# Optimization experiments

Hardware: AMD Instinct MI355X
Metric: run time of the kernel (lower is better)

## Reference

```python
import jax, jax.numpy as jnp
import numpy as np

EMBED_DIM = 1280
NUM_STATES = 20
B, L = 8, 1024

# upper-triangular (offset=1) indices, matching torch.triu_indices(N, N, offset=1)
_IU, _JU = np.triu_indices(NUM_STATES, k=1)


def setup_inputs() -> dict:
    key = jax.random.key(0)
    ks = jax.random.split(key, 4)
    d = EMBED_DIM
    n = NUM_STATES
    m = n * (n - 1) // 2
    s = 1.0 / np.sqrt(d)
    return {
        "hx": jax.random.normal(ks[0], (B, L, d), dtype=jnp.float32),
        "dense_w": jax.random.normal(ks[1], (d, d), dtype=jnp.float32) * s,
        "dense_b": jnp.zeros((d,), dtype=jnp.float32),
        "ln_w": jnp.ones((d,), dtype=jnp.float32),
        "ln_b": jnp.zeros((d,), dtype=jnp.float32),
        "theta_w": jax.random.normal(ks[2], (d, n), dtype=jnp.float32) * s,
        "theta_b": jnp.zeros((n,), dtype=jnp.float32),
        "Theta_w": jax.random.normal(ks[3], (d, m), dtype=jnp.float32) * s,
        "Theta_b": jnp.zeros((m,), dtype=jnp.float32),
    }


def _layer_norm(x, w, b, eps=1e-5):
    mu = jnp.mean(x, axis=-1, keepdims=True)
    var = jnp.mean(jnp.square(x - mu), axis=-1, keepdims=True)
    return (x - mu) * jax.lax.rsqrt(var + eps) * w + b


def reference(hx, dense_w, dense_b, ln_w, ln_b, theta_w, theta_b, Theta_w, Theta_b):
    n = NUM_STATES
    # dense -> exact gelu (ESM uses erf gelu) -> layer norm
    h = hx @ dense_w + dense_b                        # [B,L,D]
    h = _layer_norm(jax.nn.gelu(h, approximate=False), ln_w, ln_b)
    pi = jax.nn.softmax(h @ theta_w + theta_b, axis=-1)          # [B,L,N]
    Theta = jax.nn.softplus(h @ Theta_w + Theta_b)               # [B,L,N*(N-1)/2]
    # scatter upper triangle, then symmetrize
    S = jnp.zeros((*h.shape[:2], n, n), dtype=h.dtype).at[..., _IU, _JU].set(Theta)
    S = S + jnp.swapaxes(S, -2, -1)                              # [B,L,N,N]
    # diag(1/sqrt(pi)) @ S @ diag(sqrt(pi)) == elementwise row/col scaling
    pi_sqrt = jnp.sqrt(pi)
    Q = S * (pi_sqrt[..., None, :] / pi_sqrt[..., :, None])
    # Q - diag_embed(Q.sum(-1))
    Q = Q - Q.sum(axis=-1)[..., :, None] * jnp.eye(n, dtype=Q.dtype)
    return Q
```

## Files before the change

kernel.cpp:

```cpp
#include <hip/hip_runtime.h>
#include <hip/hip_bf16.h>
#include <math.h>

#define D 1280
#define NST 20
#define MTRI 190
#define NTOK 8192
#define NC 256

typedef __attribute__((ext_vector_type(4))) float f32x4;
typedef __attribute__((ext_vector_type(8))) __bf16 bf16x8;
typedef __attribute__((ext_vector_type(8))) unsigned short ushort8;
typedef __attribute__((ext_vector_type(4))) unsigned short bfu4;

__device__ __forceinline__ void gload_lds16(const void* g, void* l) {
    __builtin_amdgcn_global_load_lds(
        (const __attribute__((address_space(1))) void*)g,
        (__attribute__((address_space(3))) void*)l, 16, 0, 0);
}

__device__ __forceinline__ unsigned short f2bf(float x) {
    __hip_bfloat16 b = __float2bfloat16(x);
    return __builtin_bit_cast(unsigned short, b);
}
__device__ __forceinline__ float bf2f(unsigned short u) {
    unsigned int x = ((unsigned int)u) << 16;
    return __builtin_bit_cast(float, x);
}

__global__ __launch_bounds__(256) void tobf_kernel(
    const float* __restrict__ X, unsigned short* __restrict__ Y)
{
    const size_t i = ((size_t)blockIdx.x * 256 + threadIdx.x) * 8;
    float4 a = *(const float4*)(X + i);
    float4 b = *(const float4*)(X + i + 4);
    ushort8 u;
    u[0] = f2bf(a.x); u[1] = f2bf(a.y); u[2] = f2bf(a.z); u[3] = f2bf(a.w);
    u[4] = f2bf(b.x); u[5] = f2bf(b.y); u[6] = f2bf(b.z); u[7] = f2bf(b.w);
    *(ushort8*)(Y + i) = u;
}

__global__ __launch_bounds__(256) void transpose_w_kernel(
    const float* __restrict__ W, unsigned short* __restrict__ Wt)
{
    __shared__ float t[64][65];
    const int tid = threadIdx.x;
    const int k0 = blockIdx.x * 64, n0 = blockIdx.y * 64;
#pragma unroll
    for (int i = 0; i < 16; ++i) {
        int lin = i * 256 + tid;
        int r = lin >> 6, c = lin & 63;
        t[r][c] = W[(size_t)(k0 + r) * D + n0 + c];
    }
    __syncthreads();
#pragma unroll
    for (int i = 0; i < 16; ++i) {
        int lin = i * 256 + tid;
        int r = lin >> 6, c = lin & 63;
        Wt[(size_t)(n0 + r) * D + (k0 + c)] = f2bf(t[c][r]);
    }
}

__global__ __launch_bounds__(256) void build_wcat_kernel(
    const float* __restrict__ theta_w, const float* __restrict__ Theta_w,
    unsigned short* __restrict__ Wcat)
{
    const int col = threadIdx.x;
    const int k0  = blockIdx.x * 64;
    for (int kk = 0; kk < 64; kk += 8) {
        ushort8 u;
#pragma unroll
        for (int j = 0; j < 8; ++j) {
            int k = k0 + kk + j;
            float v = 0.0f;
            if (col < NST)             v = theta_w[(size_t)k * NST + col];
            else if (col < NST + MTRI) v = Theta_w[(size_t)k * MTRI + (col - NST)];
            u[j] = f2bf(v);
        }
        *(ushort8*)&Wcat[(size_t)col * D + k0 + kk] = u;
    }
}

#define BKA 32

__global__ __launch_bounds__(256) void gemm_gelu_mfma_kernel(
    const unsigned short* __restrict__ Ab,
    const unsigned short* __restrict__ Wt,
    const float* __restrict__ bias,
    unsigned short* __restrict__ H)
{
    __shared__ unsigned short As[2][128 * BKA];
    __shared__ unsigned short Bs[2][64 * BKA];

    const int tid  = threadIdx.x;
    const int lane = tid & 63;
    const int w    = tid >> 6;
    const int wr   = w >> 1;
    const int wc   = w & 1;

    const int bid = blockIdx.x;
    const int swz = (bid & 7) * 160 + (bid >> 3);
    const int row0 = (swz / 20) * 128;
    const int col0 = (swz % 20) * 64;

    f32x4 acc[4][2];
#pragma unroll
    for (int m = 0; m < 4; ++m)
#pragma unroll
        for (int n = 0; n < 2; ++n) acc[m][n] = (f32x4)0.0f;

    const int sR = lane >> 2;
    const int sK = (lane & 3) * 8;
    const unsigned short* aSrc = &Ab[(size_t)(row0 + w * 16 + sR) * D + sK];
    const unsigned short* bSrc = &Wt[(size_t)(col0 + w * 16 + sR) * D + sK];

    auto STAGE = [&](int b, int k0) {
#pragma unroll
        for (int p = 0; p < 2; ++p)
            gload_lds16(aSrc + (size_t)(p * 64) * D + k0, &As[b][(p * 64 + w * 16) * BKA]);
        gload_lds16(bSrc + k0, &Bs[b][(w * 16) * BKA]);
    };

    STAGE(0, 0);
    __syncthreads();

    const int fr = lane & 15;
    const int fk = (lane >> 4) * 8;

    for (int t = 0; t < 40; ++t) {
        const int cur = t & 1;
        if (t < 39) STAGE(cur ^ 1, (t + 1) * BKA);

        bf16x8 af[4], bfv[2];
#pragma unroll
        for (int m = 0; m < 4; ++m)
            af[m] = *(const bf16x8*)&As[cur][(wr * 64 + m * 16 + fr) * BKA + fk];
#pragma unroll
        for (int n = 0; n < 2; ++n)
            bfv[n] = *(const bf16x8*)&Bs[cur][(wc * 32 + n * 16 + fr) * BKA + fk];
#pragma unroll
        for (int m = 0; m < 4; ++m)
#pragma unroll
            for (int n = 0; n < 2; ++n)
                acc[m][n] = __builtin_amdgcn_mfma_f32_16x16x32_bf16(
                    af[m], bfv[n], acc[m][n], 0, 0, 0);
        __syncthreads();
    }

    const int crow = (lane >> 4) * 4;
#pragma unroll
    for (int n = 0; n < 2; ++n) {
        const int col = col0 + wc * 32 + n * 16 + fr;
        const float bv = bias[col];
#pragma unroll
        for (int m = 0; m < 4; ++m) {
            const int rbase = row0 + wr * 64 + m * 16 + crow;
#pragma unroll
            for (int r = 0; r < 4; ++r) {
                float h = acc[m][n][r] + bv;
                float g = 0.5f * h * (1.0f + erff(h * 0.70710678118654752f));
                H[(size_t)(rbase + r) * D + col] = f2bf(g);
            }
        }
    }
}

__global__ __launch_bounds__(256) void ln_stats_kernel(
    const unsigned short* __restrict__ Hb, float2* __restrict__ stats)
{
    const int wave = threadIdx.x >> 6, lane = threadIdx.x & 63;
    const int row = blockIdx.x * 4 + wave;
    const unsigned short* src = Hb + (size_t)row * D;
    float sum = 0.f, sq = 0.f;
#pragma unroll
    for (int i = 0; i < 5; ++i) {
        bfu4 u = *(const bfu4*)(src + (size_t)(i * 64 + lane) * 4);
#pragma unroll
        for (int j = 0; j < 4; ++j) {
            float f = bf2f(u[j]);
            sum += f; sq += f * f;
        }
    }
#pragma unroll
    for (int off = 1; off < 64; off <<= 1) {
        sum += __shfl_xor(sum, off);
        sq  += __shfl_xor(sq, off);
    }
    if (lane == 0) {
        float mean = sum * (1.0f / D);
        float var  = sq * (1.0f / D) - mean * mean;
        stats[row] = make_float2(mean, rsqrtf(var + 1e-5f));
    }
}

__global__ __launch_bounds__(256) void head_mfma_kernel(
    const unsigned short* __restrict__ Hb,
    const float2* __restrict__ stats,
    const float* __restrict__ ln_w, const float* __restrict__ ln_b,
    const float* __restrict__ theta_b, const float* __restrict__ Theta_b,
    const unsigned short* __restrict__ Wcat,
    float* __restrict__ Out)
{
    __shared__ unsigned short Bs[2][NC * 32];
    __shared__ unsigned short As[2][16 * 32];
    __shared__ float lnw_s[D], lnb_s[D];
    __shared__ float biascat[NC];
    __shared__ float mean_s[16], inv_s[16];
    float (*th_l)[NST]  = (float (*)[NST])&Bs[0][0];
    float (*sp_l)[MTRI] = (float (*)[MTRI])((char*)&Bs[0][0] + 16 * NST * 4);
    float (*s_l)[NST]   = (float (*)[NST])((char*)&Bs[0][0] + 16 * NST * 4 + 16 * MTRI * 4);

    const int tid  = threadIdx.x;
    const int lane = tid & 63;
    const int wave = tid >> 6;
    const int bid  = blockIdx.x;
    const int swz  = (bid & 7) * 64 + (bid >> 3);
    const int g0   = swz * 16;

#pragma unroll
    for (int i = 0; i < 5; ++i) {
        int k = i * 256 + tid;
        lnw_s[k] = ln_w[k];
        lnb_s[k] = ln_b[k];
    }
    {
        float v = 0.0f;
        if (tid < NST) v = theta_b[tid];
        else if (tid < NST + MTRI) v = Theta_b[tid - NST];
        biascat[tid] = v;
    }
    if (tid < 16) {
        float2 s = stats[g0 + tid];
        mean_s[tid] = s.x;
        inv_s[tid]  = s.y;
    }
    __syncthreads();

    auto STAGEB = [&](int b, int k0) {
#pragma unroll
        for (int i = 0; i < 4; ++i) {
            const int c0 = wave * 64 + i * 16;
            gload_lds16(&Wcat[(size_t)(c0 + (lane >> 2)) * D + k0 + (lane & 3) * 8],
                        &Bs[b][c0 * 32]);
        }
    };
    auto STAGEA = [&](int b, int k0) {
        if (lane < 16) {
            const int row = wave * 4 + (lane >> 2);
            const int k8  = (lane & 3) * 8;
            const float mean = mean_s[row], inv = inv_s[row];
            ushort8 u = *(const ushort8*)(Hb + (size_t)(g0 + row) * D + k0 + k8);
            ushort8 o;
#pragma unroll
            for (int j = 0; j < 8; ++j) {
                int k = k0 + k8 + j;
                o[j] = f2bf((bf2f(u[j]) - mean) * inv * lnw_s[k] + lnb_s[k]);
            }
            *(ushort8*)&As[b][row * 32 + k8] = o;
        }
    };

    STAGEB(0, 0);
    STAGEA(0, 0);
    __syncthreads();

    f32x4 acc[4];
#pragma unroll
    for (int n = 0; n < 4; ++n) acc[n] = (f32x4)0.0f;

    const int fr = lane & 15;
    const int fk = (lane >> 4) * 8;

    for (int t = 0; t < 40; ++t) {
        const int cur = t & 1;
        if (t < 39) {
            STAGEB(cur ^ 1, (t + 1) * 32);
            STAGEA(cur ^ 1, (t + 1) * 32);
        }
        bf16x8 af = *(const bf16x8*)&As[cur][fr * 32 + fk];
#pragma unroll
        for (int n = 0; n < 4; ++n) {
            bf16x8 bfv = *(const bf16x8*)&Bs[cur][(wave * 64 + n * 16 + fr) * 32 + fk];
            acc[n] = __builtin_amdgcn_mfma_f32_16x16x32_bf16(af, bfv, acc[n], 0, 0, 0);
        }
        __syncthreads();
    }

    const int crow = (lane >> 4) * 4;
#pragma unroll
    for (int n = 0; n < 4; ++n) {
        const int col = wave * 64 + n * 16 + fr;
        const float bv = biascat[col];
#pragma unroll
        for (int r = 0; r < 4; ++r) {
            const int row = crow + r;
            float v = acc[n][r] + bv;
            if (col < NST) {
                th_l[row][col] = v;
            } else if (col < NST + MTRI) {
                sp_l[row][col - NST] = (v > 20.0f) ? v : log1pf(expf(v));
            }
        }
    }
    __syncthreads();

#pragma unroll
    for (int p = 0; p < 2; ++p) {
        const int r = p * 8 + wave * 2 + (lane >> 5);
        const int l = lane & 31;
        float v = (l < NST) ? th_l[r][l] : -1e30f;
        float m = v;
#pragma unroll
        for (int off = 16; off >= 1; off >>= 1) m = fmaxf(m, __shfl_xor(m, off));
        float e = (l < NST) ? __expf(v - m) : 0.0f;
        float s = e;
#pragma unroll
        for (int off = 16; off >= 1; off >>= 1) s += __shfl_xor(s, off);
        if (l < NST) s_l[r][l] = sqrtf(e / s);
    }
    __syncthreads();

#pragma unroll
    for (int base = 0; base < 320; base += 256) {
        const int idx = base + tid;
        if (idx < 320) {
            const int r = idx / NST;
            const int i = idx % NST;
            const float inv_si = 1.0f / s_l[r][i];
            float q[NST];
            float rowsum = 0.f;
#pragma unroll
            for (int j = 0; j < NST; ++j) {
                if (j == i) { q[j] = 0.f; continue; }
                int a = (i < j) ? i : j;
                int b = (i < j) ? j : i;
                int tix = a * NST - a * (a + 1) / 2 + (b - a - 1);
                float v = sp_l[r][tix] * s_l[r][j] * inv_si;
                q[j] = v;
                rowsum += v;
            }
            q[i] = -rowsum;
            float* dst = Out + (size_t)(g0 + r) * (NST * NST) + i * NST;
#pragma unroll
            for (int j4 = 0; j4 < 5; ++j4) {
                *(float4*)(dst + j4 * 4) =
                    make_float4(q[j4 * 4], q[j4 * 4 + 1], q[j4 * 4 + 2], q[j4 * 4 + 3]);
            }
        }
    }
}

extern "C" void kernel_launch(void* const* d_in, const int* in_sizes, int n_in,
                              void* d_out, int out_size, void* d_ws, size_t ws_size,
                              hipStream_t stream) {
    const float* hx      = (const float*)d_in[0];
    const float* dense_w = (const float*)d_in[1];
    const float* dense_b = (const float*)d_in[2];
    const float* ln_w    = (const float*)d_in[3];
    const float* ln_b    = (const float*)d_in[4];
    const float* theta_w = (const float*)d_in[5];
    const float* theta_b = (const float*)d_in[6];
    const float* Theta_w = (const float*)d_in[7];
    const float* Theta_b = (const float*)d_in[8];
    float* out = (float*)d_out;

    unsigned short* hxb  = (unsigned short*)d_ws;
    unsigned short* H    = hxb + (size_t)NTOK * D;
    unsigned short* Wt   = H + (size_t)NTOK * D;
    unsigned short* Wcat = Wt + (size_t)D * D;
    float2* stats        = (float2*)d_ws;

    tobf_kernel<<<(NTOK * D) / 2048, 256, 0, stream>>>(hx, hxb);

    dim3 gridT(D / 64, D / 64);
    transpose_w_kernel<<<gridT, 256, 0, stream>>>(dense_w, Wt);
    build_wcat_kernel<<<D / 64, 256, 0, stream>>>(theta_w, Theta_w, Wcat);

    gemm_gelu_mfma_kernel<<<1280, 256, 0, stream>>>(hxb, Wt, dense_b, H);

    ln_stats_kernel<<<NTOK / 4, 256, 0, stream>>>(H, stats);

    head_mfma_kernel<<<512, 256, 0, stream>>>(H, stats, ln_w, ln_b, theta_b,
                                              Theta_b, Wcat, out);
}
```

Before: 128.0 us.

## Deepen GEMM LDS pipeline to 4 stages with vmcnt waits and XOR swizzle

```diff
diff --git a/kernel.cpp b/kernel.cpp
--- a/kernel.cpp
+++ b/kernel.cpp
@@ -82,6 +82,7 @@
 }
 
 #define BKA 32
+#define KITERS (D / BKA)
 
 __global__ __launch_bounds__(256) void gemm_gelu_mfma_kernel(
     const unsigned short* __restrict__ Ab,
@@ -89,8 +90,8 @@
     const float* __restrict__ bias,
     unsigned short* __restrict__ H)
 {
-    __shared__ unsigned short As[2][128 * BKA];
-    __shared__ unsigned short Bs[2][64 * BKA];
+    __shared__ unsigned short As[4][128 * BKA];
+    __shared__ unsigned short Bs[4][64 * BKA];
 
     const int tid  = threadIdx.x;
     const int lane = tid & 63;
@@ -110,27 +111,23 @@
         for (int n = 0; n < 2; ++n) acc[m][n] = (f32x4)0.0f;
 
     const int sR = lane >> 2;
-    const int sK = (lane & 3) * 8;
+    const int sK = ((lane & 3) ^ ((sR >> 1) & 3)) * 8;
     const unsigned short* aSrc = &Ab[(size_t)(row0 + w * 16 + sR) * D + sK];
     const unsigned short* bSrc = &Wt[(size_t)(col0 + w * 16 + sR) * D + sK];
 
-    auto STAGE = [&](int b, int k0) {
+    auto STAGE = [&](int b, int kt) {
+        const int k0 = kt * BKA;
 #pragma unroll
         for (int p = 0; p < 2; ++p)
-            gload_lds16(aSrc + (size_t)(p * 64) * D + k0, &As[b][(p * 64 + w * 16) * BKA]);
+            gload_lds16(aSrc + (size_t)(p * 64) * D + k0,
+                        &As[b][(p * 64 + w * 16) * BKA]);
         gload_lds16(bSrc + k0, &Bs[b][(w * 16) * BKA]);
     };
 
-    STAGE(0, 0);
-    __syncthreads();
-
     const int fr = lane & 15;
-    const int fk = (lane >> 4) * 8;
-
-    for (int t = 0; t < 40; ++t) {
-        const int cur = t & 1;
-        if (t < 39) STAGE(cur ^ 1, (t + 1) * BKA);
-
+    const int fk = (((lane >> 4) ^ ((fr >> 1) & 3))) * 8;
+
+    auto COMPUTE = [&](int cur) {
         bf16x8 af[4], bfv[2];
 #pragma unroll
         for (int m = 0; m < 4; ++m)
@@ -144,8 +141,26 @@
             for (int n = 0; n < 2; ++n)
                 acc[m][n] = __builtin_amdgcn_mfma_f32_16x16x32_bf16(
                     af[m], bfv[n], acc[m][n], 0, 0, 0);
-        __syncthreads();
-    }
+    };
+
+    STAGE(0, 0);
+    STAGE(1, 1);
+
+    for (int t = 0; t < KITERS - 2; ++t) {
+        STAGE((t + 2) & 3, t + 2);
+        asm volatile("s_waitcnt vmcnt(6)" ::: "memory");
+        __builtin_amdgcn_s_barrier();
+        asm volatile("" ::: "memory");
+        COMPUTE(t & 3);
+    }
+    asm volatile("s_waitcnt vmcnt(3)" ::: "memory");
+    __builtin_amdgcn_s_barrier();
+    asm volatile("" ::: "memory");
+    COMPUTE((KITERS - 2) & 3);
+    asm volatile("s_waitcnt vmcnt(0)" ::: "memory");
+    __builtin_amdgcn_s_barrier();
+    asm volatile("" ::: "memory");
+    COMPUTE((KITERS - 1) & 3);
 
     const int crow = (lane >> 4) * 4;
 #pragma unroll
```

New measurement: 129.9 us. About the same (+1.5%).

## Fold LayerNorm affine and normalization into head weights and epilogue

Applied to the files above, without the earlier changes.

```diff
diff --git a/kernel.cpp b/kernel.cpp
--- a/kernel.cpp
+++ b/kernel.cpp
@@ -63,6 +63,7 @@
 
 __global__ __launch_bounds__(256) void build_wcat_kernel(
     const float* __restrict__ theta_w, const float* __restrict__ Theta_w,
+    const float* __restrict__ ln_w,
     unsigned short* __restrict__ Wcat)
 {
     const int col = threadIdx.x;
@@ -75,9 +76,40 @@
             float v = 0.0f;
             if (col < NST)             v = theta_w[(size_t)k * NST + col];
             else if (col < NST + MTRI) v = Theta_w[(size_t)k * MTRI + (col - NST)];
-            u[j] = f2bf(v);
+            u[j] = f2bf(ln_w[k] * v);
         }
         *(ushort8*)&Wcat[(size_t)col * D + k0 + kk] = u;
+    }
+}
+
+__global__ __launch_bounds__(64) void build_uv_kernel(
+    const unsigned short* __restrict__ Wcat,
+    const float* __restrict__ theta_w, const float* __restrict__ Theta_w,
+    const float* __restrict__ ln_b,
+    const float* __restrict__ theta_b, const float* __restrict__ Theta_b,
+    float* __restrict__ U, float* __restrict__ Vp)
+{
+    const int col  = blockIdx.x;
+    const int lane = threadIdx.x;
+    float u = 0.f, v = 0.f;
+    for (int k = lane; k < D; k += 64) {
+        u += bf2f(Wcat[(size_t)col * D + k]);
+        float w = 0.f;
+        if (col < NST)             w = theta_w[(size_t)k * NST + col];
+        else if (col < NST + MTRI) w = Theta_w[(size_t)k * MTRI + (col - NST)];
+        v += ln_b[k] * w;
+    }
+#pragma unroll
+    for (int off = 1; off < 64; off <<= 1) {
+        u += __shfl_xor(u, off);
+        v += __shfl_xor(v, off);
+    }
+    if (lane == 0) {
+        float b = 0.f;
+        if (col < NST)             b = theta_b[col];
+        else if (col < NST + MTRI) b = Theta_b[col - NST];
+        U[col]  = u;
+        Vp[col] = v + b;
     }
 }
 
@@ -196,15 +228,13 @@
 __global__ __launch_bounds__(256) void head_mfma_kernel(
     const unsigned short* __restrict__ Hb,
     const float2* __restrict__ stats,
-    const float* __restrict__ ln_w, const float* __restrict__ ln_b,
-    const float* __restrict__ theta_b, const float* __restrict__ Theta_b,
+    const float* __restrict__ U, const float* __restrict__ Vp,
     const unsigned short* __restrict__ Wcat,
     float* __restrict__ Out)
 {
     __shared__ unsigned short Bs[2][NC * 32];
     __shared__ unsigned short As[2][16 * 32];
-    __shared__ float lnw_s[D], lnb_s[D];
-    __shared__ float biascat[NC];
+    __shared__ float U_s[NC], V_s[NC];
     __shared__ float mean_s[16], inv_s[16];
     float (*th_l)[NST]  = (float (*)[NST])&Bs[0][0];
     float (*sp_l)[MTRI] = (float (*)[MTRI])((char*)&Bs[0][0] + 16 * NST * 4);
@@ -217,24 +247,13 @@
     const int swz  = (bid & 7) * 64 + (bid >> 3);
     const int g0   = swz * 16;
 
-#pragma unroll
-    for (int i = 0; i < 5; ++i) {
-        int k = i * 256 + tid;
-        lnw_s[k] = ln_w[k];
-        lnb_s[k] = ln_b[k];
-    }
-    {
-        float v = 0.0f;
-        if (tid < NST) v = theta_b[tid];
-        else if (tid < NST + MTRI) v = Theta_b[tid - NST];
-        biascat[tid] = v;
-    }
+    U_s[tid] = U[tid];
+    V_s[tid] = Vp[tid];
     if (tid < 16) {
         float2 s = stats[g0 + tid];
         mean_s[tid] = s.x;
         inv_s[tid]  = s.y;
     }
-    __syncthreads();
 
     auto STAGEB = [&](int b, int k0) {
 #pragma unroll
@@ -245,18 +264,9 @@
         }
     };
     auto STAGEA = [&](int b, int k0) {
-        if (lane < 16) {
-            const int row = wave * 4 + (lane >> 2);
-            const int k8  = (lane & 3) * 8;
-            const float mean = mean_s[row], inv = inv_s[row];
-            ushort8 u = *(const ushort8*)(Hb + (size_t)(g0 + row) * D + k0 + k8);
-            ushort8 o;
-#pragma unroll
-            for (int j = 0; j < 8; ++j) {
-                int k = k0 + k8 + j;
-                o[j] = f2bf((bf2f(u[j]) - mean) * inv * lnw_s[k] + lnb_s[k]);
-            }
-            *(ushort8*)&As[b][row * 32 + k8] = o;
+        if (wave == 0) {
+            gload_lds16(&Hb[(size_t)(g0 + (lane >> 2)) * D + k0 + (lane & 3) * 8],
+                        &As[b][0]);
         }
     };
 
@@ -290,11 +300,12 @@
 #pragma unroll
     for (int n = 0; n < 4; ++n) {
         const int col = wave * 64 + n * 16 + fr;
-        const float bv = biascat[col];
+        const float Uc = U_s[col];
+        const float Vc = V_s[col];
 #pragma unroll
         for (int r = 0; r < 4; ++r) {
             const int row = crow + r;
-            float v = acc[n][r] + bv;
+            float v = inv_s[row] * (acc[n][r] - mean_s[row] * Uc) + Vc;
             if (col < NST) {
                 th_l[row][col] = v;
             } else if (col < NST + MTRI) {
@@ -368,18 +379,21 @@
     unsigned short* H    = hxb + (size_t)NTOK * D;
     unsigned short* Wt   = H + (size_t)NTOK * D;
     unsigned short* Wcat = Wt + (size_t)D * D;
-    float2* stats        = (float2*)d_ws;
+    float2* stats        = (float2*)(Wcat + (size_t)NC * D);
+    float* U             = (float*)(stats + NTOK);
+    float* Vp            = U + NC;
 
     tobf_kernel<<<(NTOK * D) / 2048, 256, 0, stream>>>(hx, hxb);
 
     dim3 gridT(D / 64, D / 64);
     transpose_w_kernel<<<gridT, 256, 0, stream>>>(dense_w, Wt);
-    build_wcat_kernel<<<D / 64, 256, 0, stream>>>(theta_w, Theta_w, Wcat);
+    build_wcat_kernel<<<D / 64, 256, 0, stream>>>(theta_w, Theta_w, ln_w, Wcat);
+    build_uv_kernel<<<NC, 64, 0, stream>>>(Wcat, theta_w, Theta_w, ln_b,
+                                           theta_b, Theta_b, U, Vp);
 
     gemm_gelu_mfma_kernel<<<1280, 256, 0, stream>>>(hxb, Wt, dense_b, H);
 
     ln_stats_kernel<<<NTOK / 4, 256, 0, stream>>>(H, stats);
 
-    head_mfma_kernel<<<512, 256, 0, stream>>>(H, stats, ln_w, ln_b, theta_b,
-                                              Theta_b, Wcat, out);
-}
+    head_mfma_kernel<<<512, 256, 0, stream>>>(H, stats, U, Vp, Wcat, out);
+}
```

Measured after the change: 131.6 us. 2.8% more time.
